# Kernel tuning notes

Hardware: AMD Instinct MI355X
Metric: run time of the kernel (lower is better)

The kernel has to match this reference:

```python
import jax, jax.numpy as jnp
import numpy as np

# ---- static config (from grid_conf / data_aug_conf) ----
B, N, C = 4, 6, 64            # batch, cameras, camC
OGH, OGW = 256, 704           # final_dim
DOWN = 16                     # 32 // up_scale
FH, FW = OGH // DOWN, OGW // DOWN   # 16, 44
DB0, DB1, DBS = 4.0, 45.0, 1.0      # dbound
D = int((DB1 - DB0) / DBS)          # 41 depth bins
DX = np.array([0.5, 0.5, 20.0], np.float32)            # dx
BX = np.array([-49.75, -49.75, 0.0], np.float32)        # bx (lower + dx/2)
NX = (200, 200, 1)                                       # nx


def make_frustum():
    # [D, FH, FW, 3] pixel (u, v, depth) frustum, matches torch create_frustum
    ds = jnp.arange(DB0, DB1, DBS, dtype=jnp.float32)[:, None, None] * jnp.ones((1, FH, FW), jnp.float32)
    xs = jnp.linspace(0.0, OGW - 1.0, FW, dtype=jnp.float32)[None, None, :] * jnp.ones((D, FH, 1), jnp.float32)
    ys = jnp.linspace(0.0, OGH - 1.0, FH, dtype=jnp.float32)[None, :, None] * jnp.ones((D, 1, FW), jnp.float32)
    return jnp.stack([xs, ys, ds], axis=-1)


def get_geometry(rots, trans, intrins, post_rots, post_trans):
    # frustum points -> ego frame, [B, N, D, FH, FW, 3]
    pts = make_frustum()[None, None] - post_trans[:, :, None, None, None, :]
    pts = jnp.einsum('bnij,bndhwj->bndhwi', jnp.linalg.inv(post_rots), pts)
    # un-project: (u*d, v*d, d)
    pts = jnp.concatenate([pts[..., :2] * pts[..., 2:3], pts[..., 2:3]], axis=-1)
    combine = rots @ jnp.linalg.inv(intrins)
    return jnp.einsum('bnij,bndhwj->bndhwi', combine, pts) + trans[:, :, None, None, None, :]


def voxel_pooling(geom, x):
    # geom: [B,N,D,H,W,3] ego coords; x: [B,N,D,H,W,C] lifted features
    dx = jnp.asarray(DX); bx = jnp.asarray(BX)
    # voxel indices; .astype(int32) truncates toward zero like torch .long()
    gi = ((geom - (bx - dx / 2.0)) / dx).astype(jnp.int32)
    Np = B * N * D * FH * FW
    gi = gi.reshape(Np, 3)
    xf = x.reshape(Np, C)
    bidx = jnp.repeat(jnp.arange(B, dtype=jnp.int32), N * D * FH * FW)
    valid = ((gi[:, 0] >= 0) & (gi[:, 0] < NX[0]) &
             (gi[:, 1] >= 0) & (gi[:, 1] < NX[1]) &
             (gi[:, 2] >= 0) & (gi[:, 2] < NX[2]))
    # flat voxel id: (((b*nz + z)*nx0 + xi)*nx1 + yi)
    flat = ((bidx * NX[2] + gi[:, 2]) * NX[0] + gi[:, 0]) * NX[1] + gi[:, 1]
    flat = jnp.where(valid, flat, 0)
    xf = xf * valid[:, None].astype(xf.dtype)
    nvox = B * NX[2] * NX[0] * NX[1]
    # scatter-add == sort + cumsum-trick per-voxel sum in the torch code
    final = jax.ops.segment_sum(xf, flat, num_segments=nvox)          # [nvox, C]
    final = final.reshape(B, NX[2], NX[0], NX[1], C)
    final = jnp.transpose(final, (0, 1, 4, 2, 3)).reshape(B, NX[2] * C, NX[0], NX[1])
    return final


def setup_inputs() -> dict:
    key = jax.random.key(0)
    k1, k2 = jax.random.split(key)
    feat_depth = jax.random.normal(k1, (B, N, D, FH, FW), jnp.float32)
    feat_pv = jax.random.normal(k2, (B, N, C, FH, FW), jnp.float32)
    # realistic 6-camera nuScenes-like rig, intrinsics scaled to 704x256
    base = np.array([[0., 0., 1.], [-1., 0., 0.], [0., -1., 0.]], np.float32)  # cam axes -> ego axes
    rots = np.zeros((B, N, 3, 3), np.float32)
    trans = np.zeros((B, N, 3), np.float32)
    for n in range(N):
        yaw = 2.0 * np.pi * n / N
        Rz = np.array([[np.cos(yaw), -np.sin(yaw), 0.], [np.sin(yaw), np.cos(yaw), 0.], [0., 0., 1.]], np.float32)
        rots[:, n] = Rz @ base
        trans[:, n] = Rz @ np.array([1.5, 0.0, 1.6], np.float32)
    fx = 1266.0 * (OGW / 1600.0)
    intr = np.array([[fx, 0., OGW / 2.0], [0., fx, OGH / 2.0], [0., 0., 1.]], np.float32)
    return {
        'feat_depth': feat_depth,
        'feat_pv': feat_pv,
        'rots': jnp.asarray(rots),
        'trans': jnp.asarray(trans),
        'intrins': jnp.asarray(np.broadcast_to(intr, (B, N, 3, 3)).copy()),
        'post_rots': jnp.asarray(np.broadcast_to(np.eye(3, dtype=np.float32), (B, N, 3, 3)).copy()),
        'post_trans': jnp.zeros((B, N, 3), jnp.float32),
    }


def reference(feat_depth, feat_pv, rots, trans, intrins, post_rots, post_trans):
    geom = get_geometry(rots, trans, intrins, post_rots, post_trans)
    geom = jax.lax.stop_gradient(geom)  # torch casts to .long(): indices are non-diff
    depth = jax.nn.softmax(feat_depth, axis=2)                 # get_depth_dist over D
    # lift: depth.unsqueeze(1) * feat.unsqueeze(2) -> [B,N,D,C,H,W] -> [B,N,D,H,W,C]
    x = depth[:, :, :, None] * feat_pv[:, :, None]
    x = jnp.transpose(x, (0, 1, 2, 4, 5, 3))
    return voxel_pooling(geom, x)                               # [B, C*nz, 200, 200]
```

## Files before the change

### kernel.cpp

```cpp
#include <hip/hip_runtime.h>
#include <math.h>

namespace {
constexpr int kB = 4, kN = 6, kC = 64, kD = 41, kFH = 16, kFW = 44;
constexpr int kNX0 = 200, kNX1 = 200;
constexpr int kPix = kB * kN * kFH * kFW;
constexpr int kPts = kPix * kD;
constexpr int kVox = kB * kNX0 * kNX1;
constexpr int kPvElems = kPix * kC;
constexpr int kScanBlks = kVox / 256;

constexpr size_t kOffPvT    = 0;
constexpr size_t kSzPvT     = (size_t)kPvElems * 4;
constexpr size_t kOffVox    = kOffPvT + kSzPvT;
constexpr size_t kSzVox     = (size_t)kPts * 4;
constexpr size_t kOffWgt    = kOffVox + kSzVox;
constexpr size_t kSzWgt     = (size_t)kPts * 4;
constexpr size_t kOffCnt    = kOffWgt + kSzWgt;
constexpr size_t kSzCnt     = (size_t)kVox * 4;
constexpr size_t kOffOffs   = kOffCnt + kSzCnt;
constexpr size_t kSzOffs    = 640256;
constexpr size_t kOffBSum   = kOffOffs + kSzOffs;
constexpr size_t kSzBSum    = 2560;
constexpr size_t kOffSKW    = kOffBSum + kSzBSum;
constexpr size_t kSzSKW     = (size_t)kPts * 8;
constexpr size_t kWsNeed    = kOffSKW + kSzSKW + 256;
}

__device__ __forceinline__ void inv3x3(const float m[9], float inv[9]) {
    float a = m[0], b = m[1], c = m[2];
    float d = m[3], e = m[4], f = m[5];
    float g = m[6], h = m[7], i = m[8];
    float A =  (e * i - f * h);
    float Bm = -(d * i - f * g);
    float Cm =  (d * h - e * g);
    float det = a * A + b * Bm + c * Cm;
    float r = 1.0f / det;
    inv[0] = A * r;
    inv[1] = -(b * i - c * h) * r;
    inv[2] =  (b * f - c * e) * r;
    inv[3] = Bm * r;
    inv[4] =  (a * i - c * g) * r;
    inv[5] = -(a * f - c * d) * r;
    inv[6] = Cm * r;
    inv[7] = -(a * h - b * g) * r;
    inv[8] =  (a * e - b * d) * r;
}

__global__ __launch_bounds__(256) void lss_pvt(const float* __restrict__ pv,
                                               float* __restrict__ pvT,
                                               unsigned* __restrict__ counts) {
    int i = blockIdx.x * 256 + threadIdx.x;
    if (i < kPvElems) {
        int c = i & 63;
        int pix = i >> 6;
        int bn = pix / (kFH * kFW), hw = pix % (kFH * kFW);
        pvT[i] = pv[(bn * kC + c) * (kFH * kFW) + hw];
    }
    if (i < kVox) counts[i] = 0u;
}

__global__ __launch_bounds__(256) void lss_geom(
    const float* __restrict__ feat_depth,
    const float* __restrict__ rots,
    const float* __restrict__ trans,
    const float* __restrict__ intrins,
    const float* __restrict__ post_rots,
    const float* __restrict__ post_trans,
    int* __restrict__ voxArr, float* __restrict__ wgtArr,
    unsigned* __restrict__ counts)
{
    const int lane = threadIdx.x & 63;
    const int wave = threadIdx.x >> 6;
    const int pix  = blockIdx.x * 4 + wave;

    const int w  = pix % kFW;
    const int h  = (pix / kFW) % kFH;
    const int bn = pix / (kFW * kFH);
    const int b  = bn / kN;

    const float* R  = rots       + bn * 9;
    const float* K  = intrins    + bn * 9;
    const float* PR = post_rots  + bn * 9;
    const float* PT = post_trans + bn * 3;
    const float* T  = trans      + bn * 3;

    float Km[9], PRm[9];
#pragma unroll
    for (int i = 0; i < 9; ++i) { Km[i] = K[i]; PRm[i] = PR[i]; }
    float invK[9], invPR[9];
    inv3x3(Km, invK);
    inv3x3(PRm, invPR);
    float M[9];
#pragma unroll
    for (int i = 0; i < 3; ++i)
#pragma unroll
        for (int j = 0; j < 3; ++j)
            M[i * 3 + j] = R[i * 3 + 0] * invK[0 * 3 + j]
                         + R[i * 3 + 1] * invK[1 * 3 + j]
                         + R[i * 3 + 2] * invK[2 * 3 + j];
    const float pt0 = PT[0], pt1 = PT[1], pt2 = PT[2];
    const float t0 = T[0], t1 = T[1], t2 = T[2];

    const int pixBase = h * kFW + w;
    float fd = -INFINITY;
    if (lane < kD)
        fd = feat_depth[(bn * kD + lane) * (kFH * kFW) + pixBase];
    float mx = fd;
#pragma unroll
    for (int off = 32; off >= 1; off >>= 1)
        mx = fmaxf(mx, __shfl_xor(mx, off));
    float ex = (lane < kD) ? __expf(fd - mx) : 0.0f;
    float sm = ex;
#pragma unroll
    for (int off = 32; off >= 1; off >>= 1)
        sm += __shfl_xor(sm, off);
    const float wgt = ex / sm;

    if (lane < kD) {
        const float u  = (float)w * (703.0f / 43.0f);
        const float v  = (float)h * 17.0f;
        const float dv = 4.0f + (float)lane;
        const float px = u - pt0, py = v - pt1, pz = dv - pt2;
        const float ax = invPR[0] * px + invPR[1] * py + invPR[2] * pz;
        const float ay = invPR[3] * px + invPR[4] * py + invPR[5] * pz;
        const float az = invPR[6] * px + invPR[7] * py + invPR[8] * pz;
        const float qx = ax * az, qy = ay * az, qz = az;
        const float gx = M[0] * qx + M[1] * qy + M[2] * qz + t0;
        const float gy = M[3] * qx + M[4] * qy + M[5] * qz + t1;
        const float gz = M[6] * qx + M[7] * qy + M[8] * qz + t2;
        const float fx = (gx + 50.0f) / 0.5f;
        const float fy = (gy + 50.0f) / 0.5f;
        const float fz = (gz + 10.0f) / 20.0f;
        const int gix = (int)fx;
        const int giy = (int)fy;
        const int giz = (int)fz;
        int flat = -1;
        if (gix >= 0 && gix < kNX0 && giy >= 0 && giy < kNX1 && giz == 0) {
            flat = (b * kNX0 + gix) * kNX1 + giy;
            atomicAdd(&counts[flat], 1u);
        }
        const int p = pix * kD + lane;
        voxArr[p] = flat;
        wgtArr[p] = wgt;
    }
}

__global__ __launch_bounds__(256) void lss_scan_a(const unsigned* __restrict__ counts,
                                                  unsigned* __restrict__ offsets,
                                                  unsigned* __restrict__ blockSums) {
    const int i = blockIdx.x * 256 + threadIdx.x;
    const int lane = threadIdx.x & 63;
    const int wv = threadIdx.x >> 6;
    const unsigned c = counts[i];
    unsigned s = c;
#pragma unroll
    for (int o = 1; o < 64; o <<= 1) {
        unsigned v = __shfl_up(s, o);
        if (lane >= o) s += v;
    }
    __shared__ unsigned wsum[4];
    if (lane == 63) wsum[wv] = s;
    __syncthreads();
    unsigned base = 0;
#pragma unroll
    for (int k = 0; k < 3; ++k)
        if (k < wv) base += wsum[k];
    const unsigned incl = s + base;
    offsets[i] = incl - c;
    if (threadIdx.x == 255) blockSums[blockIdx.x] = incl;
}

__global__ __launch_bounds__(1024) void lss_scan_b(unsigned* __restrict__ blockSums,
                                                   unsigned* __restrict__ offsets) {
    const int t = threadIdx.x;
    const int lane = t & 63;
    const int wv = t >> 6;
    const unsigned c = (t < kScanBlks) ? blockSums[t] : 0u;
    unsigned s = c;
#pragma unroll
    for (int o = 1; o < 64; o <<= 1) {
        unsigned v = __shfl_up(s, o);
        if (lane >= o) s += v;
    }
    __shared__ unsigned wsum[16];
    if (lane == 63) wsum[wv] = s;
    __syncthreads();
    unsigned base = 0;
#pragma unroll
    for (int k = 0; k < 15; ++k)
        if (k < wv) base += wsum[k];
    const unsigned incl = s + base;
    if (t < kScanBlks) blockSums[t] = incl - c;
    if (t == 1023) offsets[kVox] = incl;
}

__global__ __launch_bounds__(256) void lss_scan_c(const unsigned* __restrict__ blockSums,
                                                  unsigned* __restrict__ offsets) {
    const int i = blockIdx.x * 256 + threadIdx.x;
    offsets[i] += blockSums[blockIdx.x];
}

__global__ __launch_bounds__(256) void lss_order(const int* __restrict__ voxArr,
                                                 const float* __restrict__ wgtArr,
                                                 unsigned* __restrict__ offsets,
                                                 uint2* __restrict__ skw) {
    const int p = blockIdx.x * 256 + threadIdx.x;
    if (p < kPts) {
        const int f = voxArr[p];
        if (f >= 0) {
            const unsigned slot = atomicAdd(&offsets[f], 1u);
            uint2 u;
            u.x = (unsigned)(p / kD);
            u.y = __float_as_uint(wgtArr[p]);
            skw[slot] = u;
        }
    }
}

__global__ __launch_bounds__(512) void lss_gather(const float* __restrict__ pvT,
                                                  const unsigned* __restrict__ offsets,
                                                  const uint2* __restrict__ skw,
                                                  float* __restrict__ out) {
    constexpr int kChunk = 2048;
    __shared__ float acc[50][65];
    __shared__ uint2 sbuf[kChunk];
    __shared__ unsigned rowOff[51];
    const int tile = blockIdx.x;
    const int yt = tile & 3;
    const int xi = (tile >> 2) % kNX0;
    const int b  = tile / (kNX0 * 4);
    const int yi0 = yt * 50;
    const int lane = threadIdx.x & 63;
    const int wave = threadIdx.x >> 6;
    const int flat0 = (b * kNX0 + xi) * kNX1 + yi0;

    for (int e = threadIdx.x; e < 50 * 65; e += 512)
        ((float*)acc)[e] = 0.0f;
    if (threadIdx.x < 51) {
        const int f = flat0 - 1 + (int)threadIdx.x;
        rowOff[threadIdx.x] = (f < 0) ? 0u : offsets[f];
    }
    __syncthreads();

    const unsigned seg0 = rowOff[0];
    const unsigned seg1 = rowOff[50];

    for (unsigned cb = seg0; cb < seg1; cb += (unsigned)kChunk) {
        const unsigned ce = min(cb + (unsigned)kChunk, seg1);
        const int n = (int)(ce - cb);
        for (int e = threadIdx.x; e < n; e += 512)
            sbuf[e] = skw[cb + e];
        __syncthreads();

        for (int j = wave; j < 50; j += 8) {
            unsigned s0 = max(rowOff[j], cb);
            unsigned e0 = min(rowOff[j + 1], ce);
            if (s0 >= e0) continue;
            float a0 = 0.0f, a1 = 0.0f, a2 = 0.0f, a3 = 0.0f;
            int p  = (int)(s0 - cb);
            int pe = (int)(e0 - cb);
            for (; p + 4 <= pe; p += 4) {
                const uint2 u0 = sbuf[p + 0];
                const uint2 u1 = sbuf[p + 1];
                const uint2 u2 = sbuf[p + 2];
                const uint2 u3 = sbuf[p + 3];
                a0 += __uint_as_float(u0.y) * pvT[u0.x * kC + lane];
                a1 += __uint_as_float(u1.y) * pvT[u1.x * kC + lane];
                a2 += __uint_as_float(u2.y) * pvT[u2.x * kC + lane];
                a3 += __uint_as_float(u3.y) * pvT[u3.x * kC + lane];
            }
            for (; p < pe; ++p) {
                const uint2 u = sbuf[p];
                a0 += __uint_as_float(u.y) * pvT[u.x * kC + lane];
            }
            acc[j][lane] += (a0 + a1) + (a2 + a3);
        }
        __syncthreads();
    }
    __syncthreads();

    for (int e = threadIdx.x; e < kC * 50; e += 512) {
        const int c = e / 50, j = e % 50;
        out[((b * kC + c) * (kNX0 * kNX1)) + xi * kNX1 + yi0 + j] = acc[j][c];
    }
}

__global__ __launch_bounds__(256) void lss_scatter_fb(
    const float* __restrict__ feat_depth,
    const float* __restrict__ feat_pv,
    const float* __restrict__ rots,
    const float* __restrict__ trans,
    const float* __restrict__ intrins,
    const float* __restrict__ post_rots,
    const float* __restrict__ post_trans,
    float* __restrict__ out)
{
    const int lane = threadIdx.x & 63;
    const int wave = threadIdx.x >> 6;
    const int pix  = blockIdx.x * 4 + wave;
    const int w  = pix % kFW;
    const int h  = (pix / kFW) % kFH;
    const int bn = pix / (kFW * kFH);
    const int b  = bn / kN;
    const float* R  = rots       + bn * 9;
    const float* K  = intrins    + bn * 9;
    const float* PR = post_rots  + bn * 9;
    const float* PT = post_trans + bn * 3;
    const float* T  = trans      + bn * 3;
    float Km[9], PRm[9];
#pragma unroll
    for (int i = 0; i < 9; ++i) { Km[i] = K[i]; PRm[i] = PR[i]; }
    float invK[9], invPR[9];
    inv3x3(Km, invK);
    inv3x3(PRm, invPR);
    float M[9];
#pragma unroll
    for (int i = 0; i < 3; ++i)
#pragma unroll
        for (int j = 0; j < 3; ++j)
            M[i * 3 + j] = R[i * 3 + 0] * invK[0 * 3 + j]
                         + R[i * 3 + 1] * invK[1 * 3 + j]
                         + R[i * 3 + 2] * invK[2 * 3 + j];
    const float pt0 = PT[0], pt1 = PT[1], pt2 = PT[2];
    const float t0 = T[0], t1 = T[1], t2 = T[2];
    const int pixBase = h * kFW + w;
    float fd = -INFINITY;
    if (lane < kD)
        fd = feat_depth[(bn * kD + lane) * (kFH * kFW) + pixBase];
    float mx = fd;
#pragma unroll
    for (int off = 32; off >= 1; off >>= 1)
        mx = fmaxf(mx, __shfl_xor(mx, off));
    float ex = (lane < kD) ? __expf(fd - mx) : 0.0f;
    float sm = ex;
#pragma unroll
    for (int off = 32; off >= 1; off >>= 1)
        sm += __shfl_xor(sm, off);
    const float wgt = ex / sm;
    int vox = -1;
    if (lane < kD) {
        const float u  = (float)w * (703.0f / 43.0f);
        const float v  = (float)h * 17.0f;
        const float dv = 4.0f + (float)lane;
        const float px = u - pt0, py = v - pt1, pz = dv - pt2;
        const float ax = invPR[0] * px + invPR[1] * py + invPR[2] * pz;
        const float ay = invPR[3] * px + invPR[4] * py + invPR[5] * pz;
        const float az = invPR[6] * px + invPR[7] * py + invPR[8] * pz;
        const float qx = ax * az, qy = ay * az, qz = az;
        const float gx = M[0] * qx + M[1] * qy + M[2] * qz + t0;
        const float gy = M[3] * qx + M[4] * qy + M[5] * qz + t1;
        const float gz = M[6] * qx + M[7] * qy + M[8] * qz + t2;
        const float fx = (gx + 50.0f) / 0.5f;
        const float fy = (gy + 50.0f) / 0.5f;
        const float fz = (gz + 10.0f) / 20.0f;
        const int gix = (int)fx;
        const int giy = (int)fy;
        const int giz = (int)fz;
        if (gix >= 0 && gix < kNX0 && giy >= 0 && giy < kNX1 && giz == 0)
            vox = gix * kNX1 + giy;
    }
    const float fc = feat_pv[(bn * kC + lane) * (kFH * kFW) + pixBase];
    const int outBase = (b * kC + lane) * (kNX0 * kNX1);
#pragma unroll 1
    for (int d = 0; d < kD; ++d) {
        const int   vd = __shfl(vox, d);
        const float wd = __shfl(wgt, d);
        if (vd >= 0)
            atomicAdd(&out[outBase + vd], wd * fc);
    }
}

extern "C" void kernel_launch(void* const* d_in, const int* in_sizes, int n_in,
                              void* d_out, int out_size, void* d_ws, size_t ws_size,
                              hipStream_t stream) {
    const float* feat_depth = (const float*)d_in[0];
    const float* feat_pv    = (const float*)d_in[1];
    const float* rots       = (const float*)d_in[2];
    const float* trans      = (const float*)d_in[3];
    const float* intrins    = (const float*)d_in[4];
    const float* post_rots  = (const float*)d_in[5];
    const float* post_trans = (const float*)d_in[6];
    float* out = (float*)d_out;

    if (ws_size < kWsNeed) {
        hipMemsetAsync(out, 0, (size_t)out_size * sizeof(float), stream);
        lss_scatter_fb<<<kPix / 4, 256, 0, stream>>>(
            feat_depth, feat_pv, rots, trans, intrins, post_rots, post_trans, out);
        return;
    }

    char* ws = (char*)d_ws;
    float*    pvT      = (float*)   (ws + kOffPvT);
    int*      voxArr   = (int*)     (ws + kOffVox);
    float*    wgtArr   = (float*)   (ws + kOffWgt);
    unsigned* counts   = (unsigned*)(ws + kOffCnt);
    unsigned* offsets  = (unsigned*)(ws + kOffOffs);
    unsigned* blockSums= (unsigned*)(ws + kOffBSum);
    uint2*    skw      = (uint2*)   (ws + kOffSKW);

    lss_pvt<<<(kPvElems + 255) / 256, 256, 0, stream>>>(feat_pv, pvT, counts);
    lss_geom<<<kPix / 4, 256, 0, stream>>>(
        feat_depth, rots, trans, intrins, post_rots, post_trans,
        voxArr, wgtArr, counts);
    lss_scan_a<<<kScanBlks, 256, 0, stream>>>(counts, offsets, blockSums);
    lss_scan_b<<<1, 1024, 0, stream>>>(blockSums, offsets);
    lss_scan_c<<<kScanBlks, 256, 0, stream>>>(blockSums, offsets);
    lss_order<<<kPts / 256, 256, 0, stream>>>(voxArr, wgtArr, offsets, skw);
    lss_gather<<<kB * kNX0 * 4, 512, 0, stream>>>(pvT, offsets, skw, out);
}
```

Before: 133.7 us.

## Split geometry/softmax kernels, tile pv transpose via LDS, use depth-major point order

Replaces the per-pixel wave kernel, which idled 23 of 64 lanes, with two kernels. One does the depth softmax with one thread per pixel. The other computes voxel indices with one thread per point, ordered depth-major so neighbouring threads touch neighbouring pixels. The feat_pv transpose now goes through a padded shared-memory tile so both reads and writes are coalesced. The point order change reorders the atomic slot assignment, and the extra kernel launch adds a little overhead.

```diff
diff --git a/kernel.cpp b/kernel.cpp
--- a/kernel.cpp
+++ b/kernel.cpp
@@ -4,11 +4,13 @@
 namespace {
 constexpr int kB = 4, kN = 6, kC = 64, kD = 41, kFH = 16, kFW = 44;
 constexpr int kNX0 = 200, kNX1 = 200;
-constexpr int kPix = kB * kN * kFH * kFW;
+constexpr int kHW  = kFH * kFW;
+constexpr int kPix = kB * kN * kHW;
 constexpr int kPts = kPix * kD;
 constexpr int kVox = kB * kNX0 * kNX1;
 constexpr int kPvElems = kPix * kC;
 constexpr int kScanBlks = kVox / 256;
+constexpr int kPvtTiles = kPix / 64;
 
 constexpr size_t kOffPvT    = 0;
 constexpr size_t kSzPvT     = (size_t)kPvElems * 4;
@@ -50,34 +52,72 @@
 __global__ __launch_bounds__(256) void lss_pvt(const float* __restrict__ pv,
                                                float* __restrict__ pvT,
                                                unsigned* __restrict__ counts) {
-    int i = blockIdx.x * 256 + threadIdx.x;
-    if (i < kPvElems) {
-        int c = i & 63;
-        int pix = i >> 6;
-        int bn = pix / (kFH * kFW), hw = pix % (kFH * kFW);
-        pvT[i] = pv[(bn * kC + c) * (kFH * kFW) + hw];
-    }
-    if (i < kVox) counts[i] = 0u;
-}
-
-__global__ __launch_bounds__(256) void lss_geom(
-    const float* __restrict__ feat_depth,
+    __shared__ float t[64][65];
+    const int blk = blockIdx.x;
+    const int tid = threadIdx.x;
+    const int ci = blk * 256 + tid;
+    if (ci < kVox) counts[ci] = 0u;
+
+    if (blk < kPvtTiles) {
+        const int pix0 = blk * 64;
+        const int bn  = pix0 / kHW;
+        const int hw0 = pix0 - bn * kHW;
+        const int lane = tid & 63;
+        const int wv   = tid >> 6;
+        const float* src = pv + (size_t)(bn * kC) * kHW + hw0;
+#pragma unroll
+        for (int cc = 0; cc < 16; ++cc) {
+            const int c = wv * 16 + cc;
+            t[c][lane] = src[(size_t)c * kHW + lane];
+        }
+        __syncthreads();
+        float* dst = pvT + (size_t)pix0 * kC;
+#pragma unroll
+        for (int jj = 0; jj < 16; ++jj) {
+            const int j = wv * 16 + jj;
+            dst[j * kC + lane] = t[lane][j];
+        }
+    }
+}
+
+__global__ __launch_bounds__(256) void lss_sm(const float* __restrict__ feat_depth,
+                                              float* __restrict__ wgtArr) {
+    const int pix = blockIdx.x * 256 + threadIdx.x;
+    const int bn = pix / kHW;
+    const int hw = pix - bn * kHW;
+    const float* p = feat_depth + (size_t)(bn * kD) * kHW + hw;
+    float v[kD];
+#pragma unroll
+    for (int d = 0; d < kD; ++d) v[d] = p[(size_t)d * kHW];
+    float mx = v[0];
+#pragma unroll
+    for (int d = 1; d < kD; ++d) mx = fmaxf(mx, v[d]);
+    float sm = 0.0f;
+#pragma unroll
+    for (int d = 0; d < kD; ++d) { v[d] = __expf(v[d] - mx); sm += v[d]; }
+    const float inv = 1.0f / sm;
+    float* o = wgtArr + (size_t)(bn * kD) * kHW + hw;
+#pragma unroll
+    for (int d = 0; d < kD; ++d) o[(size_t)d * kHW] = v[d] * inv;
+}
+
+__global__ __launch_bounds__(256) void lss_geo(
     const float* __restrict__ rots,
     const float* __restrict__ trans,
     const float* __restrict__ intrins,
     const float* __restrict__ post_rots,
     const float* __restrict__ post_trans,
-    int* __restrict__ voxArr, float* __restrict__ wgtArr,
+    int* __restrict__ voxArr,
     unsigned* __restrict__ counts)
 {
-    const int lane = threadIdx.x & 63;
-    const int wave = threadIdx.x >> 6;
-    const int pix  = blockIdx.x * 4 + wave;
-
-    const int w  = pix % kFW;
-    const int h  = (pix / kFW) % kFH;
-    const int bn = pix / (kFW * kFH);
-    const int b  = bn / kN;
+    const int q   = blockIdx.x * 256 + threadIdx.x;
+    const int bn  = q / (kD * kHW);
+    const int rem = q - bn * (kD * kHW);
+    const int d   = rem / kHW;
+    const int hw  = rem - d * kHW;
+    const int h   = hw / kFW;
+    const int w   = hw - h * kFW;
+    const int b   = bn / kN;
 
     const float* R  = rots       + bn * 9;
     const float* K  = intrins    + bn * 9;
@@ -99,51 +139,30 @@
             M[i * 3 + j] = R[i * 3 + 0] * invK[0 * 3 + j]
                          + R[i * 3 + 1] * invK[1 * 3 + j]
                          + R[i * 3 + 2] * invK[2 * 3 + j];
-    const float pt0 = PT[0], pt1 = PT[1], pt2 = PT[2];
-    const float t0 = T[0], t1 = T[1], t2 = T[2];
-
-    const int pixBase = h * kFW + w;
-    float fd = -INFINITY;
-    if (lane < kD)
-        fd = feat_depth[(bn * kD + lane) * (kFH * kFW) + pixBase];
-    float mx = fd;
-#pragma unroll
-    for (int off = 32; off >= 1; off >>= 1)
-        mx = fmaxf(mx, __shfl_xor(mx, off));
-    float ex = (lane < kD) ? __expf(fd - mx) : 0.0f;
-    float sm = ex;
-#pragma unroll
-    for (int off = 32; off >= 1; off >>= 1)
-        sm += __shfl_xor(sm, off);
-    const float wgt = ex / sm;
-
-    if (lane < kD) {
-        const float u  = (float)w * (703.0f / 43.0f);
-        const float v  = (float)h * 17.0f;
-        const float dv = 4.0f + (float)lane;
-        const float px = u - pt0, py = v - pt1, pz = dv - pt2;
-        const float ax = invPR[0] * px + invPR[1] * py + invPR[2] * pz;
-        const float ay = invPR[3] * px + invPR[4] * py + invPR[5] * pz;
-        const float az = invPR[6] * px + invPR[7] * py + invPR[8] * pz;
-        const float qx = ax * az, qy = ay * az, qz = az;
-        const float gx = M[0] * qx + M[1] * qy + M[2] * qz + t0;
-        const float gy = M[3] * qx + M[4] * qy + M[5] * qz + t1;
-        const float gz = M[6] * qx + M[7] * qy + M[8] * qz + t2;
-        const float fx = (gx + 50.0f) / 0.5f;
-        const float fy = (gy + 50.0f) / 0.5f;
-        const float fz = (gz + 10.0f) / 20.0f;
-        const int gix = (int)fx;
-        const int giy = (int)fy;
-        const int giz = (int)fz;
-        int flat = -1;
-        if (gix >= 0 && gix < kNX0 && giy >= 0 && giy < kNX1 && giz == 0) {
-            flat = (b * kNX0 + gix) * kNX1 + giy;
-            atomicAdd(&counts[flat], 1u);
-        }
-        const int p = pix * kD + lane;
-        voxArr[p] = flat;
-        wgtArr[p] = wgt;
-    }
+
+    const float u  = (float)w * (703.0f / 43.0f);
+    const float v  = (float)h * 17.0f;
+    const float dv = 4.0f + (float)d;
+    const float px = u - PT[0], py = v - PT[1], pz = dv - PT[2];
+    const float ax = invPR[0] * px + invPR[1] * py + invPR[2] * pz;
+    const float ay = invPR[3] * px + invPR[4] * py + invPR[5] * pz;
+    const float az = invPR[6] * px + invPR[7] * py + invPR[8] * pz;
+    const float qx = ax * az, qy = ay * az, qz = az;
+    const float gx = M[0] * qx + M[1] * qy + M[2] * qz + T[0];
+    const float gy = M[3] * qx + M[4] * qy + M[5] * qz + T[1];
+    const float gz = M[6] * qx + M[7] * qy + M[8] * qz + T[2];
+    const float fx = (gx + 50.0f) / 0.5f;
+    const float fy = (gy + 50.0f) / 0.5f;
+    const float fz = (gz + 10.0f) / 20.0f;
+    const int gix = (int)fx;
+    const int giy = (int)fy;
+    const int giz = (int)fz;
+    int flat = -1;
+    if (gix >= 0 && gix < kNX0 && giy >= 0 && giy < kNX1 && giz == 0) {
+        flat = (b * kNX0 + gix) * kNX1 + giy;
+        atomicAdd(&counts[flat], 1u);
+    }
+    voxArr[q] = flat;
 }
 
 __global__ __launch_bounds__(256) void lss_scan_a(const unsigned* __restrict__ counts,
@@ -205,16 +224,17 @@
                                                  const float* __restrict__ wgtArr,
                                                  unsigned* __restrict__ offsets,
                                                  uint2* __restrict__ skw) {
-    const int p = blockIdx.x * 256 + threadIdx.x;
-    if (p < kPts) {
-        const int f = voxArr[p];
-        if (f >= 0) {
-            const unsigned slot = atomicAdd(&offsets[f], 1u);
-            uint2 u;
-            u.x = (unsigned)(p / kD);
-            u.y = __float_as_uint(wgtArr[p]);
-            skw[slot] = u;
-        }
+    const int q = blockIdx.x * 256 + threadIdx.x;
+    const int f = voxArr[q];
+    if (f >= 0) {
+        const unsigned slot = atomicAdd(&offsets[f], 1u);
+        const int bn  = q / (kD * kHW);
+        const int rem = q - bn * (kD * kHW);
+        const int hw  = rem % kHW;
+        uint2 u;
+        u.x = (unsigned)(bn * kHW + hw);
+        u.y = __float_as_uint(wgtArr[q]);
+        skw[slot] = u;
     }
 }
 
@@ -301,7 +321,7 @@
     const int pix  = blockIdx.x * 4 + wave;
     const int w  = pix % kFW;
     const int h  = (pix / kFW) % kFH;
-    const int bn = pix / (kFW * kFH);
+    const int bn = pix / kHW;
     const int b  = bn / kN;
     const float* R  = rots       + bn * 9;
     const float* K  = intrins    + bn * 9;
@@ -327,7 +347,7 @@
     const int pixBase = h * kFW + w;
     float fd = -INFINITY;
     if (lane < kD)
-        fd = feat_depth[(bn * kD + lane) * (kFH * kFW) + pixBase];
+        fd = feat_depth[(bn * kD + lane) * kHW + pixBase];
     float mx = fd;
 #pragma unroll
     for (int off = 32; off >= 1; off >>= 1)
@@ -360,7 +380,7 @@
         if (gix >= 0 && gix < kNX0 && giy >= 0 && giy < kNX1 && giz == 0)
             vox = gix * kNX1 + giy;
     }
-    const float fc = feat_pv[(bn * kC + lane) * (kFH * kFW) + pixBase];
+    const float fc = feat_pv[(bn * kC + lane) * kHW + pixBase];
     const int outBase = (b * kC + lane) * (kNX0 * kNX1);
 #pragma unroll 1
     for (int d = 0; d < kD; ++d) {
@@ -399,10 +419,10 @@
     unsigned* blockSums= (unsigned*)(ws + kOffBSum);
     uint2*    skw      = (uint2*)   (ws + kOffSKW);
 
-    lss_pvt<<<(kPvElems + 255) / 256, 256, 0, stream>>>(feat_pv, pvT, counts);
-    lss_geom<<<kPix / 4, 256, 0, stream>>>(
-        feat_depth, rots, trans, intrins, post_rots, post_trans,
-        voxArr, wgtArr, counts);
+    lss_pvt<<<kScanBlks, 256, 0, stream>>>(feat_pv, pvT, counts);
+    lss_sm<<<kPix / 256, 256, 0, stream>>>(feat_depth, wgtArr);
+    lss_geo<<<kPts / 256, 256, 0, stream>>>(
+        rots, trans, intrins, post_rots, post_trans, voxArr, counts);
     lss_scan_a<<<kScanBlks, 256, 0, stream>>>(counts, offsets, blockSums);
     lss_scan_b<<<1, 1024, 0, stream>>>(blockSums, offsets);
     lss_scan_c<<<kScanBlks, 256, 0, stream>>>(blockSums, offsets);
```

Result: faster. 117.9 us (-11.8%).
